# Optimization experiments

Measured on AMD Instinct MI355X. Metric: run time of the kernel, lower is better.

The kernel has to match this reference:

```python
import jax, jax.numpy as jnp
import numpy as np

N_NODES = 100000
N_EDGES = 1600000
F_IN = 128
EMB = 128
HEADS = 4
D_HEAD = EMB // HEADS
HIDDEN = 256
BATCH = 2048
CANDS = 16  # distractors + 1


def setup_inputs() -> dict:
    key = jax.random.key(0)
    ks = jax.random.split(key, 10)
    message = jax.random.normal(ks[0], (BATCH, HIDDEN), jnp.float32)
    x = jax.random.normal(ks[1], (N_NODES, F_IN), jnp.float32)
    edge_index = jax.random.randint(ks[2], (2, N_EDGES), 0, N_NODES, jnp.int64)
    indices = jax.random.randint(ks[3], (BATCH * CANDS,), 0, N_NODES, jnp.int64)
    s = 1.0 / np.sqrt(F_IN)
    W = jax.random.normal(ks[4], (F_IN, HEADS, D_HEAD), jnp.float32) * s
    att_src = jax.random.normal(ks[5], (HEADS, D_HEAD), jnp.float32) * s
    att_dst = jax.random.normal(ks[6], (HEADS, D_HEAD), jnp.float32) * s
    bias = jnp.zeros((EMB,), jnp.float32)
    fc_w = jax.random.normal(ks[7], (EMB, HIDDEN), jnp.float32) / np.sqrt(HIDDEN)
    fc_b = jnp.zeros((EMB,), jnp.float32)
    return {"message": message, "x": x, "edge_index": edge_index, "indices": indices,
            "W": W, "att_src": att_src, "att_dst": att_dst, "bias": bias,
            "fc_w": fc_w, "fc_b": fc_b}


def _gat(x, edge_index, W, att_src, att_dst, bias):
    N = x.shape[0]
    loops = jnp.arange(N, dtype=edge_index.dtype)
    src = jnp.concatenate([edge_index[0], loops])  # self-loops (PyG default)
    dst = jnp.concatenate([edge_index[1], loops])
    Wx = jnp.einsum('nf,fhd->nhd', x, W)                      # [N,H,D]
    a_s = (Wx * att_src).sum(-1)                              # [N,H]
    a_d = (Wx * att_dst).sum(-1)
    e = jax.nn.leaky_relu(a_s[src] + a_d[dst], 0.2)           # [E,H]
    m = jax.ops.segment_max(e, dst, num_segments=N)           # segment softmax
    ex = jnp.exp(e - m[dst])
    den = jax.ops.segment_sum(ex, dst, num_segments=N)
    alpha = ex / den[dst]
    out = jax.ops.segment_sum(alpha[:, :, None] * Wx[src], dst, num_segments=N)
    return out.reshape(N, -1) + bias                          # [N, H*D]


def reference(message, x, edge_index, indices, W, att_src, att_dst, bias, fc_w, fc_b):
    h = _gat(x, edge_index, W, att_src, att_dst, bias)        # [N, EMB]
    B = message.shape[0]
    emb = h[indices].reshape(B, -1, h.shape[-1])              # [B,C,EMB]
    msg = message @ fc_w.T + fc_b                             # [B,EMB]
    dots = jnp.einsum('bce,be->bc', emb, msg)                 # bmm scoring
    amax = jnp.abs(dots).max()
    tie = ((jnp.abs(dots) - amax) < 1e-10).astype(dots.dtype)
    noise = jax.random.normal(jax.random.key(42), dots.shape, dots.dtype)
    dots = dots + tie * amax * 1e-5 * noise
    return jax.nn.log_softmax(dots, axis=1)
```

## Files before the change

### kernel.cpp

```cpp
#include <hip/hip_runtime.h>
#include <stdint.h>
#include <stddef.h>

#define N_NODES 100000
#define N_EDGES 1600000
#define F_IN 128
#define EMB 128
#define HEADS 4
#define D_HEAD 32
#define HIDDEN 256
#define BATCH 2048
#define CANDS 16
#define NSLOTS 32768
#define WXBLOCKS 391
#define WTROWS 144
#define STR 136

typedef __attribute__((ext_vector_type(8))) short v8s;
typedef __attribute__((ext_vector_type(4))) float v4f;

__device__ __forceinline__ unsigned short f2bs(float f) {
  unsigned int u = __builtin_bit_cast(unsigned int, f);
  u = (u + 0x7fffu + ((u >> 16) & 1u)) >> 16;
  return (unsigned short)u;
}
__device__ __forceinline__ float bs2f(unsigned int s) {
  unsigned int u = (s & 0xffffu) << 16;
  return __builtin_bit_cast(float, u);
}

__global__ __launch_bounds__(256) void k_prep(const float* __restrict__ W,
                                              const float* __restrict__ att_src,
                                              const float* __restrict__ att_dst,
                                              unsigned short* __restrict__ Wtp,
                                              const int* __restrict__ idx,
                                              int* __restrict__ nidx,
                                              int* __restrict__ cnt) {
  int i = blockIdx.x * 256 + threadIdx.x;
  if (i < 128 * STR) {
    int r = i / STR, c = i - r * STR;
    Wtp[i] = (c < 128) ? f2bs(W[c * 128 + r]) : (unsigned short)0;
  } else if (i < WTROWS * STR) {
    int ii = i - 128 * STR;
    int r = ii / STR, c = ii - r * STR;
    unsigned short v = 0;
    if (c < 128 && r < 8) {
      const float* att = (r < 4) ? att_src : att_dst;
      int hh = r & 3;
      float s = 0.f;
#pragma unroll
      for (int d = 0; d < 32; ++d) s += W[c * 128 + hh * 32 + d] * att[hh * 32 + d];
      v = f2bs(s);
    }
    Wtp[i] = v;
  }
  if (i < NSLOTS) {
    cnt[i] = 0;
    nidx[idx[i]] = i;
  }
}

__global__ __launch_bounds__(256) void k_scatmsg(const int* __restrict__ ei,
                                                 const int* __restrict__ idx,
                                                 const int* __restrict__ nidx,
                                                 int* __restrict__ cnt,
                                                 int* __restrict__ srclist,
                                                 const float* __restrict__ message,
                                                 const float* __restrict__ fc_w,
                                                 const float* __restrict__ fc_b,
                                                 float* __restrict__ msg) {
  __shared__ float Sm[8][256];
  __shared__ float red[8 * 128];
  int tid = threadIdx.x;
  if (blockIdx.x < 256) {
    int b0 = blockIdx.x * 8;
    for (int i = tid; i < 8 * 256; i += 256)
      Sm[i >> 8][i & 255] = message[(size_t)b0 * 256 + i];
    __syncthreads();
    int e = tid & 127, half = tid >> 7;
    float acc[8];
#pragma unroll
    for (int r = 0; r < 8; ++r) acc[r] = 0.f;
    const float* wrow = fc_w + (size_t)e * 256 + half * 128;
    for (int k = 0; k < 128; k += 4) {
      float4 w4 = *(const float4*)(wrow + k);
#pragma unroll
      for (int r = 0; r < 8; ++r) {
        float4 m4 = *(const float4*)(&Sm[r][half * 128 + k]);
        acc[r] += m4.x * w4.x + m4.y * w4.y + m4.z * w4.z + m4.w * w4.w;
      }
    }
    __syncthreads();
    if (half == 0) {
#pragma unroll
      for (int r = 0; r < 8; ++r) red[r * 128 + e] = acc[r];
    }
    __syncthreads();
    if (half == 1) {
#pragma unroll
      for (int r = 0; r < 8; ++r) red[r * 128 + e] += acc[r];
    }
    __syncthreads();
    for (int i = tid; i < 1024; i += 256)
      msg[(size_t)b0 * 128 + i] = red[i] + fc_b[i & 127];
  } else {
    int e = (blockIdx.x - 256) * 256 + tid;
    if (e >= N_EDGES) return;
    int dst = ei[N_EDGES + e];
    unsigned int ni = (unsigned int)nidx[dst];
    if (ni >= NSLOTS) return;
    if (idx[ni] != dst) return;
    int pos = atomicAdd(&cnt[ni], 1);
    if (pos < 64) srclist[ni * 64 + pos] = ei[e];
  }
}

__global__ __launch_bounds__(256) void k_wx(const float* __restrict__ x,
                                            const unsigned short* __restrict__ Wtp,
                                            unsigned short* __restrict__ Wx,
                                            float* __restrict__ a_s,
                                            float* __restrict__ a_d) {
  __shared__ unsigned short wt[WTROWS * STR];
  __shared__ unsigned short xs[64 * STR];
  int tid = threadIdx.x;

  {
    const uint4* s = (const uint4*)Wtp;
    uint4* d = (uint4*)wt;
#pragma unroll
    for (int it = 0; it < 10; ++it) {
      int i = it * 256 + tid;
      if (i < WTROWS * STR / 8) d[i] = s[i];
    }
  }
  __syncthreads();

  int w = tid >> 6, lane = tid & 63;
  int m = lane & 15, quad = lane >> 4;

  for (int chunk = 0; chunk < 4; ++chunk) {
    int rbase = blockIdx.x * 256 + chunk * 64;
    int gr = rbase + w * 16 + m;
    if (gr >= N_NODES) gr = N_NODES - 1;
    const float* xrow = x + (size_t)gr * 128;

    v8s afrag[4];
#pragma unroll
    for (int t = 0; t < 4; ++t) {
      const float4* gp = (const float4*)(xrow + t * 32 + quad * 8);
      float4 f0 = gp[0], f1 = gp[1];
      v8s a;
      a[0] = (short)f2bs(f0.x); a[1] = (short)f2bs(f0.y);
      a[2] = (short)f2bs(f0.z); a[3] = (short)f2bs(f0.w);
      a[4] = (short)f2bs(f1.x); a[5] = (short)f2bs(f1.y);
      a[6] = (short)f2bs(f1.z); a[7] = (short)f2bs(f1.w);
      afrag[t] = a;
    }

    v4f acc[9];
#pragma unroll
    for (int nt = 0; nt < 9; ++nt) {
      v4f a0 = {0.f, 0.f, 0.f, 0.f};
      const unsigned short* brow = wt + (size_t)(nt * 16 + m) * STR;
#pragma unroll
      for (int t = 0; t < 4; ++t) {
        v8s b = *(const v8s*)(brow + t * 32 + quad * 8);
        a0 = __builtin_amdgcn_mfma_f32_16x16x32_bf16(afrag[t], b, a0, 0, 0, 0);
      }
      acc[nt] = a0;
    }

#pragma unroll
    for (int r = 0; r < 4; ++r) {
      int orow = rbase + w * 16 + quad * 4 + r;
      if (orow < N_NODES) {
        if (m < 4) a_s[(size_t)orow * 4 + m] = acc[8][r];
        else if (m < 8) a_d[(size_t)orow * 4 + m - 4] = acc[8][r];
      }
    }

#pragma unroll
    for (int nt = 0; nt < 8; ++nt)
#pragma unroll
      for (int r = 0; r < 4; ++r)
        xs[(w * 16 + quad * 4 + r) * STR + nt * 16 + m] = f2bs(acc[nt][r]);
    asm volatile("s_waitcnt lgkmcnt(0)" ::: "memory");
#pragma unroll
    for (int j = 0; j < 4; ++j) {
      int fr = 4 * j + (lane >> 4);
      int fc = (lane & 15) * 8;
      int grow = rbase + w * 16 + fr;
      v8s v = *(const v8s*)(&xs[(w * 16 + fr) * STR + fc]);
      if (grow < N_NODES) *(v8s*)(&Wx[(size_t)grow * 128 + fc]) = v;
    }
  }
}

__global__ __launch_bounds__(256) void k_aggscore(const float* __restrict__ a_s,
                                                  const float* __restrict__ a_d,
                                                  const unsigned short* __restrict__ Wx,
                                                  const int* __restrict__ idx,
                                                  const int* __restrict__ nidx,
                                                  const int* __restrict__ cnt,
                                                  const int* __restrict__ srclist,
                                                  const int* __restrict__ ei,
                                                  const float* __restrict__ bias,
                                                  const float* __restrict__ msg,
                                                  float* __restrict__ out) {
  __shared__ int sS[16][64];
  __shared__ float sW[16][64 * 4];
  __shared__ float sdots[16];
  int w = threadIdx.x >> 6, lane = threadIdx.x & 63;
  int q = lane >> 4, li = lane & 15;
  int wq = w * 4 + q;
  int b = blockIdx.x;
  int wid = b * 16 + wq;
  int dst = idx[wid];
  int ci = nidx[dst];
  int degRaw = cnt[ci];
  int deg = degRaw < 64 ? degRaw : 64;
  float4 ad4 = *(const float4*)(a_d + (size_t)dst * 4);
  float4 dsum = {0.f, 0.f, 0.f, 0.f};
  for (int t = li; t < deg; t += 16) {
    int sv = srclist[ci * 64 + t];
    float4 as = *(const float4*)(a_s + (size_t)sv * 4);
    float e0 = as.x + ad4.x; e0 = e0 > 0.f ? e0 : 0.2f * e0;
    float e1 = as.y + ad4.y; e1 = e1 > 0.f ? e1 : 0.2f * e1;
    float e2 = as.z + ad4.z; e2 = e2 > 0.f ? e2 : 0.2f * e2;
    float e3 = as.w + ad4.w; e3 = e3 > 0.f ? e3 : 0.2f * e3;
    float4 w4;
    w4.x = __expf(e0); w4.y = __expf(e1);
    w4.z = __expf(e2); w4.w = __expf(e3);
    sS[wq][t] = sv;
    *(float4*)(&sW[wq][t * 4]) = w4;
    dsum.x += w4.x; dsum.y += w4.y; dsum.z += w4.z; dsum.w += w4.w;
  }
  asm volatile("s_waitcnt lgkmcnt(0)" ::: "memory");

#pragma unroll
  for (int o = 8; o >= 1; o >>= 1) {
    dsum.x += __shfl_xor(dsum.x, o);
    dsum.y += __shfl_xor(dsum.y, o);
    dsum.z += __shfl_xor(dsum.z, o);
    dsum.w += __shfl_xor(dsum.w, o);
  }

  int hh = li >> 2;
  float4 as4 = *(const float4*)(a_s + (size_t)dst * 4);
  float s0 = as4.x + ad4.x; s0 = s0 > 0.f ? s0 : 0.2f * s0;
  float s1 = as4.y + ad4.y; s1 = s1 > 0.f ? s1 : 0.2f * s1;
  float s2 = as4.z + ad4.z; s2 = s2 > 0.f ? s2 : 0.2f * s2;
  float s3 = as4.w + ad4.w; s3 = s3 > 0.f ? s3 : 0.2f * s3;
  float w0 = __expf(s0), w1 = __expf(s1), w2 = __expf(s2), w3 = __expf(s3);
  float wSelf = hh < 2 ? (hh == 0 ? w0 : w1) : (hh == 2 ? w2 : w3);
  float denE = hh < 2 ? (hh == 0 ? dsum.x : dsum.y) : (hh == 2 ? dsum.z : dsum.w);
  float den = denE + wSelf;

  float acc[8];
  {
    uint4 u = *(const uint4*)(Wx + (size_t)dst * 128 + li * 8);
    acc[0] = wSelf * bs2f(u.x); acc[1] = wSelf * bs2f(u.x >> 16);
    acc[2] = wSelf * bs2f(u.y); acc[3] = wSelf * bs2f(u.y >> 16);
    acc[4] = wSelf * bs2f(u.z); acc[5] = wSelf * bs2f(u.z >> 16);
    acc[6] = wSelf * bs2f(u.w); acc[7] = wSelf * bs2f(u.w >> 16);
  }

  if (degRaw > 64) {
    float adH = hh < 2 ? (hh == 0 ? ad4.x : ad4.y) : (hh == 2 ? ad4.z : ad4.w);
    den = wSelf;
    for (int e = 0; e < N_EDGES; ++e) {
      if (ei[N_EDGES + e] == dst) {
        int sv = ei[e];
        float ash = a_s[(size_t)sv * 4 + hh];
        float ee = ash + adH; ee = ee > 0.f ? ee : 0.2f * ee;
        float wA = __expf(ee);
        den += wA;
        uint4 u = *(const uint4*)(Wx + (size_t)sv * 128 + li * 8);
        acc[0] += wA * bs2f(u.x); acc[1] += wA * bs2f(u.x >> 16);
        acc[2] += wA * bs2f(u.y); acc[3] += wA * bs2f(u.y >> 16);
        acc[4] += wA * bs2f(u.z); acc[5] += wA * bs2f(u.z >> 16);
        acc[6] += wA * bs2f(u.w); acc[7] += wA * bs2f(u.w >> 16);
      }
    }
  } else {
#pragma unroll 4
    for (int j = 0; j < deg; ++j) {
      int s = sS[wq][j];
      float wA = sW[wq][j * 4 + hh];
      uint4 u = *(const uint4*)(Wx + (size_t)s * 128 + li * 8);
      acc[0] += wA * bs2f(u.x); acc[1] += wA * bs2f(u.x >> 16);
      acc[2] += wA * bs2f(u.y); acc[3] += wA * bs2f(u.y >> 16);
      acc[4] += wA * bs2f(u.z); acc[5] += wA * bs2f(u.z >> 16);
      acc[6] += wA * bs2f(u.w); acc[7] += wA * bs2f(u.w >> 16);
    }
  }

  float inv = 1.0f / den;
  float4 b0 = *(const float4*)(bias + li * 8);
  float4 b1 = *(const float4*)(bias + li * 8 + 4);
  const float* mrow = msg + (size_t)b * 128 + li * 8;
  float4 m0 = *(const float4*)(mrow);
  float4 m1 = *(const float4*)(mrow + 4);
  float dp = (acc[0] * inv + b0.x) * m0.x + (acc[1] * inv + b0.y) * m0.y
           + (acc[2] * inv + b0.z) * m0.z + (acc[3] * inv + b0.w) * m0.w
           + (acc[4] * inv + b1.x) * m1.x + (acc[5] * inv + b1.y) * m1.y
           + (acc[6] * inv + b1.z) * m1.z + (acc[7] * inv + b1.w) * m1.w;
#pragma unroll
  for (int o = 8; o >= 1; o >>= 1) dp += __shfl_xor(dp, o);
  if (li == 0) sdots[wq] = dp;
  __syncthreads();
  if (threadIdx.x < 16) {
    float d = sdots[threadIdx.x];
    float mx = d;
#pragma unroll
    for (int o = 1; o < 16; o <<= 1) mx = fmaxf(mx, __shfl_xor(mx, o));
    float ex = __expf(d - mx);
    float sum = ex;
#pragma unroll
    for (int o = 1; o < 16; o <<= 1) sum += __shfl_xor(sum, o);
    out[b * 16 + threadIdx.x] = d - mx - __logf(sum);
  }
}

extern "C" void kernel_launch(void* const* d_in, const int* in_sizes, int n_in,
                              void* d_out, int out_size, void* d_ws, size_t ws_size,
                              hipStream_t stream) {
  (void)in_sizes; (void)n_in; (void)out_size; (void)ws_size;
  const float* message = (const float*)d_in[0];
  const float* x       = (const float*)d_in[1];
  const int*   ei      = (const int*)d_in[2];
  const int*   indices = (const int*)d_in[3];
  const float* W       = (const float*)d_in[4];
  const float* att_src = (const float*)d_in[5];
  const float* att_dst = (const float*)d_in[6];
  const float* bias    = (const float*)d_in[7];
  const float* fc_w    = (const float*)d_in[8];
  const float* fc_b    = (const float*)d_in[9];
  float* out = (float*)d_out;

  char* p = (char*)d_ws;
  auto alloc = [&](size_t bytes) -> char* {
    char* r = p;
    p += (bytes + 255) & ~(size_t)255;
    return r;
  };
  unsigned short* Wx = (unsigned short*)alloc((size_t)N_NODES * 128 * 2);
  float* a_s = (float*)alloc((size_t)N_NODES * 4 * 4);
  float* a_d = (float*)alloc((size_t)N_NODES * 4 * 4);
  unsigned short* Wtp = (unsigned short*)alloc((size_t)WTROWS * STR * 2);
  int* nidx      = (int*)alloc((size_t)N_NODES * 4);
  int* cnt       = (int*)alloc((size_t)NSLOTS * 4);
  int* srclist   = (int*)alloc((size_t)NSLOTS * 64 * 4);
  float* msg     = (float*)alloc((size_t)BATCH * 128 * 4);

  k_prep<<<128, 256, 0, stream>>>(W, att_src, att_dst, Wtp, indices, nidx, cnt);
  k_scatmsg<<<256 + N_EDGES / 256, 256, 0, stream>>>(ei, indices, nidx, cnt, srclist,
                                                     message, fc_w, fc_b, msg);
  k_wx<<<WXBLOCKS, 256, 0, stream>>>(x, Wtp, Wx, a_s, a_d);
  k_aggscore<<<BATCH, 256, 0, stream>>>(a_s, a_d, Wx, indices, nidx, cnt, srclist,
                                        ei, bias, msg, out);
}
```

Before: 180.9 us.

## Interleave Wx column layout to drop LDS transpose and halve rows per block

The Wx projection kernel now writes each row's MFMA outputs directly as interleaved columns, with column nt*16+m stored at m*8+nt. This removes the shared-memory staging buffer and transpose. It also processes 128 rows per block instead of 256, doubling the block count. The aggregation kernel is adapted so each lane's 8 values span all four heads, using per-head weights and denominators, a float4 read of the per-edge weights from LDS, and an unpermuted index for bias and message. This cuts LDS traffic and raises occupancy in exchange for narrower global stores and more exp and reciprocal work per lane.

```diff
diff --git a/kernel.cpp b/kernel.cpp
--- a/kernel.cpp
+++ b/kernel.cpp
@@ -12,7 +12,7 @@
 #define BATCH 2048
 #define CANDS 16
 #define NSLOTS 32768
-#define WXBLOCKS 391
+#define WXBLOCKS 782
 #define WTROWS 144
 #define STR 136
 
@@ -121,7 +121,6 @@
                                             float* __restrict__ a_s,
                                             float* __restrict__ a_d) {
   __shared__ unsigned short wt[WTROWS * STR];
-  __shared__ unsigned short xs[64 * STR];
   int tid = threadIdx.x;
 
   {
@@ -138,8 +137,8 @@
   int w = tid >> 6, lane = tid & 63;
   int m = lane & 15, quad = lane >> 4;
 
-  for (int chunk = 0; chunk < 4; ++chunk) {
-    int rbase = blockIdx.x * 256 + chunk * 64;
+  for (int chunk = 0; chunk < 2; ++chunk) {
+    int rbase = blockIdx.x * 128 + chunk * 64;
     int gr = rbase + w * 16 + m;
     if (gr >= N_NODES) gr = N_NODES - 1;
     const float* xrow = x + (size_t)gr * 128;
@@ -176,22 +175,11 @@
       if (orow < N_NODES) {
         if (m < 4) a_s[(size_t)orow * 4 + m] = acc[8][r];
         else if (m < 8) a_d[(size_t)orow * 4 + m - 4] = acc[8][r];
+        v8s v;
+#pragma unroll
+        for (int nt = 0; nt < 8; ++nt) v[nt] = (short)f2bs(acc[nt][r]);
+        *(v8s*)(&Wx[(size_t)orow * 128 + m * 8]) = v;
       }
-    }
-
-#pragma unroll
-    for (int nt = 0; nt < 8; ++nt)
-#pragma unroll
-      for (int r = 0; r < 4; ++r)
-        xs[(w * 16 + quad * 4 + r) * STR + nt * 16 + m] = f2bs(acc[nt][r]);
-    asm volatile("s_waitcnt lgkmcnt(0)" ::: "memory");
-#pragma unroll
-    for (int j = 0; j < 4; ++j) {
-      int fr = 4 * j + (lane >> 4);
-      int fc = (lane & 15) * 8;
-      int grow = rbase + w * 16 + fr;
-      v8s v = *(const v8s*)(&xs[(w * 16 + fr) * STR + fc]);
-      if (grow < N_NODES) *(v8s*)(&Wx[(size_t)grow * 128 + fc]) = v;
     }
   }
 }
@@ -245,66 +233,71 @@
     dsum.w += __shfl_xor(dsum.w, o);
   }
 
-  int hh = li >> 2;
   float4 as4 = *(const float4*)(a_s + (size_t)dst * 4);
   float s0 = as4.x + ad4.x; s0 = s0 > 0.f ? s0 : 0.2f * s0;
   float s1 = as4.y + ad4.y; s1 = s1 > 0.f ? s1 : 0.2f * s1;
   float s2 = as4.z + ad4.z; s2 = s2 > 0.f ? s2 : 0.2f * s2;
   float s3 = as4.w + ad4.w; s3 = s3 > 0.f ? s3 : 0.2f * s3;
-  float w0 = __expf(s0), w1 = __expf(s1), w2 = __expf(s2), w3 = __expf(s3);
-  float wSelf = hh < 2 ? (hh == 0 ? w0 : w1) : (hh == 2 ? w2 : w3);
-  float denE = hh < 2 ? (hh == 0 ? dsum.x : dsum.y) : (hh == 2 ? dsum.z : dsum.w);
-  float den = denE + wSelf;
+  float wself[4];
+  wself[0] = __expf(s0); wself[1] = __expf(s1);
+  wself[2] = __expf(s2); wself[3] = __expf(s3);
+  float den4[4];
+  den4[0] = dsum.x + wself[0]; den4[1] = dsum.y + wself[1];
+  den4[2] = dsum.z + wself[2]; den4[3] = dsum.w + wself[3];
 
   float acc[8];
   {
     uint4 u = *(const uint4*)(Wx + (size_t)dst * 128 + li * 8);
-    acc[0] = wSelf * bs2f(u.x); acc[1] = wSelf * bs2f(u.x >> 16);
-    acc[2] = wSelf * bs2f(u.y); acc[3] = wSelf * bs2f(u.y >> 16);
-    acc[4] = wSelf * bs2f(u.z); acc[5] = wSelf * bs2f(u.z >> 16);
-    acc[6] = wSelf * bs2f(u.w); acc[7] = wSelf * bs2f(u.w >> 16);
+    acc[0] = wself[0] * bs2f(u.x); acc[1] = wself[0] * bs2f(u.x >> 16);
+    acc[2] = wself[1] * bs2f(u.y); acc[3] = wself[1] * bs2f(u.y >> 16);
+    acc[4] = wself[2] * bs2f(u.z); acc[5] = wself[2] * bs2f(u.z >> 16);
+    acc[6] = wself[3] * bs2f(u.w); acc[7] = wself[3] * bs2f(u.w >> 16);
   }
 
   if (degRaw > 64) {
-    float adH = hh < 2 ? (hh == 0 ? ad4.x : ad4.y) : (hh == 2 ? ad4.z : ad4.w);
-    den = wSelf;
+    den4[0] = wself[0]; den4[1] = wself[1];
+    den4[2] = wself[2]; den4[3] = wself[3];
     for (int e = 0; e < N_EDGES; ++e) {
       if (ei[N_EDGES + e] == dst) {
         int sv = ei[e];
-        float ash = a_s[(size_t)sv * 4 + hh];
-        float ee = ash + adH; ee = ee > 0.f ? ee : 0.2f * ee;
-        float wA = __expf(ee);
-        den += wA;
+        float4 as = *(const float4*)(a_s + (size_t)sv * 4);
+        float e0 = as.x + ad4.x; e0 = e0 > 0.f ? e0 : 0.2f * e0;
+        float e1 = as.y + ad4.y; e1 = e1 > 0.f ? e1 : 0.2f * e1;
+        float e2 = as.z + ad4.z; e2 = e2 > 0.f ? e2 : 0.2f * e2;
+        float e3 = as.w + ad4.w; e3 = e3 > 0.f ? e3 : 0.2f * e3;
+        float wa0 = __expf(e0), wa1 = __expf(e1);
+        float wa2 = __expf(e2), wa3 = __expf(e3);
+        den4[0] += wa0; den4[1] += wa1; den4[2] += wa2; den4[3] += wa3;
         uint4 u = *(const uint4*)(Wx + (size_t)sv * 128 + li * 8);
-        acc[0] += wA * bs2f(u.x); acc[1] += wA * bs2f(u.x >> 16);
-        acc[2] += wA * bs2f(u.y); acc[3] += wA * bs2f(u.y >> 16);
-        acc[4] += wA * bs2f(u.z); acc[5] += wA * bs2f(u.z >> 16);
-        acc[6] += wA * bs2f(u.w); acc[7] += wA * bs2f(u.w >> 16);
+        acc[0] += wa0 * bs2f(u.x); acc[1] += wa0 * bs2f(u.x >> 16);
+        acc[2] += wa1 * bs2f(u.y); acc[3] += wa1 * bs2f(u.y >> 16);
+        acc[4] += wa2 * bs2f(u.z); acc[5] += wa2 * bs2f(u.z >> 16);
+        acc[6] += wa3 * bs2f(u.w); acc[7] += wa3 * bs2f(u.w >> 16);
       }
     }
   } else {
 #pragma unroll 4
     for (int j = 0; j < deg; ++j) {
       int s = sS[wq][j];
-      float wA = sW[wq][j * 4 + hh];
+      float4 wv = *(const float4*)(&sW[wq][j * 4]);
       uint4 u = *(const uint4*)(Wx + (size_t)s * 128 + li * 8);
-      acc[0] += wA * bs2f(u.x); acc[1] += wA * bs2f(u.x >> 16);
-      acc[2] += wA * bs2f(u.y); acc[3] += wA * bs2f(u.y >> 16);
-      acc[4] += wA * bs2f(u.z); acc[5] += wA * bs2f(u.z >> 16);
-      acc[6] += wA * bs2f(u.w); acc[7] += wA * bs2f(u.w >> 16);
-    }
-  }
-
-  float inv = 1.0f / den;
-  float4 b0 = *(const float4*)(bias + li * 8);
-  float4 b1 = *(const float4*)(bias + li * 8 + 4);
-  const float* mrow = msg + (size_t)b * 128 + li * 8;
-  float4 m0 = *(const float4*)(mrow);
-  float4 m1 = *(const float4*)(mrow + 4);
-  float dp = (acc[0] * inv + b0.x) * m0.x + (acc[1] * inv + b0.y) * m0.y
-           + (acc[2] * inv + b0.z) * m0.z + (acc[3] * inv + b0.w) * m0.w
-           + (acc[4] * inv + b1.x) * m1.x + (acc[5] * inv + b1.y) * m1.y
-           + (acc[6] * inv + b1.z) * m1.z + (acc[7] * inv + b1.w) * m1.w;
+      acc[0] += wv.x * bs2f(u.x); acc[1] += wv.x * bs2f(u.x >> 16);
+      acc[2] += wv.y * bs2f(u.y); acc[3] += wv.y * bs2f(u.y >> 16);
+      acc[4] += wv.z * bs2f(u.z); acc[5] += wv.z * bs2f(u.z >> 16);
+      acc[6] += wv.w * bs2f(u.w); acc[7] += wv.w * bs2f(u.w >> 16);
+    }
+  }
+
+  float invh[4];
+  invh[0] = 1.0f / den4[0]; invh[1] = 1.0f / den4[1];
+  invh[2] = 1.0f / den4[2]; invh[3] = 1.0f / den4[3];
+  const float* mrow = msg + (size_t)b * 128;
+  float dp = 0.f;
+#pragma unroll
+  for (int k = 0; k < 8; ++k) {
+    int c = k * 16 + li;
+    dp += (acc[k] * invh[k >> 1] + bias[c]) * mrow[c];
+  }
 #pragma unroll
   for (int o = 8; o >= 1; o >>= 1) dp += __shfl_xor(dp, o);
   if (li == 0) sdots[wq] = dp;
```

Result: slower. 186.7 us (+3.2%).
